# Performance work log

Measured on AMD Instinct MI355X. Metric: run time of the kernel, lower is better.

Reference implementation:

```python
import jax, jax.numpy as jnp
import numpy as np
from jax import lax

N_CLASS, SOS, EOS, NEG = 5, 0, 4, -10000.0


def _lstm_dir(x, Wih, Whh, bih, bhh, reverse):
    # x: (T, B, Din); PyTorch gate order i, f, g, o
    T, B, _ = x.shape
    Hd = Whh.shape[1]
    h0 = jnp.zeros((B, Hd), x.dtype)

    def step(carry, xt):
        h, c = carry
        g = xt @ Wih.T + h @ Whh.T + bih + bhh
        i, f, gg, o = jnp.split(g, 4, axis=-1)
        c = jax.nn.sigmoid(f) * c + jax.nn.sigmoid(i) * jnp.tanh(gg)
        h = jax.nn.sigmoid(o) * jnp.tanh(c)
        return (h, c), h

    xs = x[::-1] if reverse else x
    _, hs = lax.scan(step, (h0, h0), xs)
    return hs[::-1] if reverse else hs


def _forward(input_ids, tags, mask, emb, convs, lstm_params, lin_w, lin_b, transition):
    T, B = mask.shape
    x = emb[input_ids][:, None]  # (N, 1, L, E)
    pooled = []
    for w, b in convs:  # w: (K, 1, size, E)
        c = lax.conv_general_dilated(x, w, (1, 1), 'VALID',
                                     dimension_numbers=('NCHW', 'OIHW', 'NCHW'))
        c = jax.nn.relu(c[..., 0] + b[None, :, None])  # (N, K, L-size+1)
        pooled.append(jnp.max(c, axis=2))              # max-pool over length
    para = jnp.concatenate(pooled, axis=1)             # (N, 3K)
    h = para.reshape(B, T, -1).transpose(1, 0, 2)      # (T, B, 3K); equal para_len
    for (Wf, Uf, bf, cf, Wb, Ub, bb, cb) in lstm_params:  # 2-layer BiLSTM (eval: no dropout)
        hf = _lstm_dir(h, Wf, Uf, bf, cf, False)
        hb = _lstm_dir(h, Wb, Ub, bb, cb, True)
        h = jnp.concatenate([hf, hb], axis=-1)
    m = mask[..., None]
    feats = ((h * m) @ lin_w.T + lin_b) * m            # (T, B, 5)

    # CRF forward algorithm (log partition)
    alpha0 = jnp.full((B, N_CLASS), NEG, feats.dtype).at[:, SOS].set(0.0)

    def step(alpha, inp):
        feat, mt = inp
        s = alpha[:, None, :] + transition[None] + feat[:, :, None]
        new = jax.nn.logsumexp(s, axis=-1)
        return new * mt[:, None] + alpha * (1.0 - mt[:, None]), None

    alpha, _ = lax.scan(step, alpha0, (feats, mask))
    fwd_score = jax.nn.logsumexp(alpha + transition[EOS][None], axis=-1)

    # gold path score
    tags_ext = jnp.concatenate([jnp.full((1, B), SOS, tags.dtype), tags], 0)  # (T+1, B)
    emit = jnp.take_along_axis(feats, tags[..., None], axis=-1)[..., 0]       # (T, B)
    trans = transition[tags_ext[1:], tags_ext[:-1]]                           # (T, B)
    gold = jnp.sum((emit + trans) * mask, axis=0)
    lengths = mask.sum(0).astype(jnp.int32)
    last = tags_ext[lengths, jnp.arange(B)]
    gold = gold + transition[EOS, last]
    return (fwd_score - gold).sum()


def setup_inputs() -> dict:
    key = jax.random.key(0)
    ks = jax.random.split(key, 32)
    B, T, L, V, E, K, H = 8, 64, 64, 50000, 768, 256, 64
    N = B * T
    inp = {}
    inp['input_ids'] = jax.random.randint(ks[0], (N, L), 1, V)
    inp['tags'] = jax.random.randint(ks[1], (T, B), 1, 4)  # B/I/O tags
    inp['mask'] = jnp.ones((T, B), jnp.float32)
    inp['para_len'] = jnp.full((B,), T, jnp.int32)
    inp['emb'] = jax.random.normal(ks[2], (V, E)) * 0.1
    for i, sz in enumerate((3, 4, 5)):
        inp[f'cw{sz}'] = jax.random.normal(ks[3 + i], (K, 1, sz, E)) * (1.0 / np.sqrt(sz * E))
        inp[f'cb{sz}'] = jnp.zeros((K,), jnp.float32)
    kidx = 6
    for layer, din in ((0, 3 * K), (1, 2 * H)):
        for d in 'fb':
            inp[f'Wih{layer}{d}'] = jax.random.normal(ks[kidx], (4 * H, din)) * (1.0 / np.sqrt(din)); kidx += 1
            inp[f'Whh{layer}{d}'] = jax.random.normal(ks[kidx], (4 * H, H)) * (1.0 / np.sqrt(H)); kidx += 1
            inp[f'bih{layer}{d}'] = jnp.zeros((4 * H,), jnp.float32)
            inp[f'bhh{layer}{d}'] = jnp.zeros((4 * H,), jnp.float32)
    inp['lin_w'] = jax.random.normal(ks[kidx], (N_CLASS, 2 * H)) * 0.1; kidx += 1
    inp['lin_b'] = jnp.zeros((N_CLASS,), jnp.float32)
    tr = jax.random.normal(ks[kidx], (N_CLASS, N_CLASS))
    inp['transition'] = tr.at[SOS, :].set(NEG).at[:, EOS].set(NEG)
    return inp


def reference(input_ids, tags, mask, para_len, emb, cw3, cb3, cw4, cb4, cw5, cb5,
              Wih0f, Whh0f, bih0f, bhh0f, Wih0b, Whh0b, bih0b, bhh0b,
              Wih1f, Whh1f, bih1f, bhh1f, Wih1b, Whh1b, bih1b, bhh1b,
              lin_w, lin_b, transition):
    convs = ((cw3, cb3), (cw4, cb4), (cw5, cb5))
    lstm_params = ((Wih0f, Whh0f, bih0f, bhh0f, Wih0b, Whh0b, bih0b, bhh0b),
                   (Wih1f, Whh1f, bih1f, bhh1f, Wih1b, Whh1b, bih1b, bhh1b))
    return _forward(input_ids, tags, mask, emb, convs, lstm_params, lin_w, lin_b, transition)
```

## Files before the change

### kernel.cpp

```cpp
#include <hip/hip_runtime.h>
#include <cstdint>
#include <cstddef>

#define DEV __device__ __forceinline__

typedef __bf16 bf16x8 __attribute__((ext_vector_type(8)));
typedef float f32x4 __attribute__((ext_vector_type(4)));

#define NEG_VAL -10000.0f

DEV unsigned int f2bf(float f) {
    unsigned int u = __float_as_uint(f);
    return (u + 0x7FFFu + ((u >> 16) & 1u)) >> 16;
}
DEV unsigned int pk2(float a, float b) { return f2bf(a) | (f2bf(b) << 16); }

DEV float sigf(float x)  { return __builtin_amdgcn_rcpf(1.f + __expf(-x)); }
DEV float tanhff(float x){ return 2.f * __builtin_amdgcn_rcpf(1.f + __expf(-2.f * x)) - 1.f; }

__global__ void cast_all_kernel(const float* __restrict__ cw3,
                                const float* __restrict__ cw4,
                                const float* __restrict__ cw5,
                                const float* __restrict__ Wih0f,
                                const float* __restrict__ Wih0b,
                                const float* __restrict__ Wih1f,
                                const float* __restrict__ Wih1b,
                                unsigned short* __restrict__ wbc,
                                unsigned short* __restrict__ wih0c,
                                unsigned short* __restrict__ wih1c) {
    int tid = blockIdx.x * blockDim.x + threadIdx.x;
    const float* src;
    uint4* dstp;
    if (tid < 294912) {
        int g   = tid & 3;
        int col = (tid >> 2) & 255;
        int c   = (tid >> 10) % 24;
        int p   = tid / (24 * 256 * 4);
        int sz, j; const float* W;
        if (p < 3)      { sz = 3; j = p;     W = cw3; }
        else if (p < 7) { sz = 4; j = p - 3; W = cw4; }
        else            { sz = 5; j = p - 7; W = cw5; }
        src = W + ((size_t)col * sz + j) * 768 + c * 32 + g * 8;
        dstp = reinterpret_cast<uint4*>(wbc) +
               ((size_t)(p * 24 + c) * 1024 + (col >> 4) * 64 + g * 16 + (col & 15));
    } else if (tid < 294912 + 49152) {
        int u   = tid - 294912;
        int g   = u & 3;
        int col = (u >> 2) & 255;
        int kc  = (u >> 10) % 24;
        int dir = u / (24 * 256 * 4);
        const float* W = dir ? Wih0b : Wih0f;
        src = W + (size_t)col * 768 + kc * 32 + g * 8;
        dstp = reinterpret_cast<uint4*>(wih0c) +
               ((size_t)(dir * 24 + kc) * 1024 + (col >> 4) * 64 + g * 16 + (col & 15));
    } else if (tid < 294912 + 49152 + 8192) {
        int u   = tid - 294912 - 49152;
        int g   = u & 3;
        int col = (u >> 2) & 255;
        int kc  = (u >> 10) % 4;
        int dir = u / (4 * 256 * 4);
        const float* W = dir ? Wih1b : Wih1f;
        src = W + (size_t)col * 128 + kc * 32 + g * 8;
        dstp = reinterpret_cast<uint4*>(wih1c) +
               ((size_t)(dir * 4 + kc) * 1024 + (col >> 4) * 64 + g * 16 + (col & 15));
    } else return;
    float4 a = *(const float4*)(src);
    float4 b = *(const float4*)(src + 4);
    *dstp = make_uint4(pk2(a.x, a.y), pk2(a.z, a.w), pk2(b.x, b.y), pk2(b.z, b.w));
}

template<int SZ>
DEV void conv_body(const int* __restrict__ ids,
                   const float* __restrict__ emb,
                   const unsigned short* __restrict__ wbc,
                   const float* __restrict__ cb,
                   unsigned short* __restrict__ para_bf,
                   int pair, int szi, int pbase,
                   unsigned short* Xlds)
{
    int tid  = threadIdx.x;
    int lane = tid & 63;
    int nw   = tid >> 6;
    int l15  = lane & 15;
    int q    = lane >> 4;
    int n0   = pair * 2;

    int srow  = tid >> 1;
    int shalf = tid & 1;
    int sid   = ids[(n0 + (srow >> 6)) * 64 + (srow & 63)];
    const float* embrow = emb + (size_t)sid * 768 + shalf * 16;
    int skey = (srow >> 1) & 3;
    int xo0 = srow * 32 + (((2 * shalf)     ^ skey) * 8);
    int xo1 = srow * 32 + (((2 * shalf + 1) ^ skey) * 8);

    int vlaneB = nw * 2048 + lane * 8;

    f32x4 acc[8][4];
    #pragma unroll
    for (int a = 0; a < 8; a++)
        #pragma unroll
        for (int t = 0; t < 4; t++) acc[a][t] = (f32x4){0.f, 0.f, 0.f, 0.f};

    bf16x8 bfr[2][4];
    float4 e0, e1, e2, e3;

    {
        e0 = ((const float4*)embrow)[0];
        e1 = ((const float4*)embrow)[1];
        e2 = ((const float4*)embrow)[2];
        e3 = ((const float4*)embrow)[3];
        const unsigned short* bt = wbc + (size_t)(pbase * 24) * 8192 + vlaneB;
        #pragma unroll
        for (int t = 0; t < 4; t++)
            bfr[0][t] = *(const bf16x8*)(bt + t * 512);
        uint4 p0 = make_uint4(pk2(e0.x, e0.y), pk2(e0.z, e0.w),
                              pk2(e1.x, e1.y), pk2(e1.z, e1.w));
        uint4 p1 = make_uint4(pk2(e2.x, e2.y), pk2(e2.z, e2.w),
                              pk2(e3.x, e3.y), pk2(e3.z, e3.w));
        *(uint4*)&Xlds[xo0] = p0;
        *(uint4*)&Xlds[xo1] = p1;
        asm volatile("s_waitcnt lgkmcnt(0)" ::: "memory");
        __builtin_amdgcn_s_barrier();
    }

    int cbase = pbase * 24;
    for (int c2 = 0; c2 < 24; c2 += 2, cbase += 2) {
        #pragma unroll
        for (int s2 = 0; s2 < 2 * SZ; ++s2) {
            const int half = (s2 < SZ) ? 0 : 1;
            const int j    = s2 - half * SZ;
            const int par  = s2 & 1;
            {
                const int sP = s2 + 1;
                const int offP = (sP < SZ) ? sP * 24
                               : (sP < 2 * SZ ? (sP - SZ) * 24 + 1 : 2);
                const unsigned short* bt =
                    wbc + (size_t)(cbase + offP) * 8192 + vlaneB;
                #pragma unroll
                for (int t = 0; t < 4; t++)
                    bfr[par ^ 1][t] = *(const bf16x8*)(bt + t * 512);
            }
            if (s2 == 0 || s2 == SZ) {
                int cE = half ? c2 + 2 : c2 + 1; if (cE > 23) cE = 0;
                const float* sp = embrow + cE * 32;
                e0 = ((const float4*)sp)[0];
                e1 = ((const float4*)sp)[1];
                e2 = ((const float4*)sp)[2];
                e3 = ((const float4*)sp)[3];
            }

            const unsigned short* Xb = Xlds + half * 4096;
            {
                bf16x8 af[4];
                #pragma unroll
                for (int a = 0; a < 4; a++) {
                    int pp = 16 * a + l15 + j; if (pp > 63) pp = 63;
                    af[a] = *(const bf16x8*)(
                        &Xb[pp * 32 + ((q ^ ((pp >> 1) & 3)) * 8)]);
                }
                __builtin_amdgcn_s_setprio(1);
                #pragma unroll
                for (int a = 0; a < 4; a++)
                    #pragma unroll
                    for (int t = 0; t < 4; t++)
                        acc[a][t] = __builtin_amdgcn_mfma_f32_16x16x32_bf16(
                            af[a], bfr[par][t], acc[a][t], 0, 0, 0);
                __builtin_amdgcn_s_setprio(0);
            }
            {
                bf16x8 af[4];
                #pragma unroll
                for (int a = 0; a < 4; a++) {
                    int pp = 16 * a + l15 + j; if (pp > 63) pp = 63;
                    int xr = 64 + pp;
                    af[a] = *(const bf16x8*)(
                        &Xb[xr * 32 + ((q ^ ((xr >> 1) & 3)) * 8)]);
                }
                __builtin_amdgcn_s_setprio(1);
                #pragma unroll
                for (int a = 0; a < 4; a++)
                    #pragma unroll
                    for (int t = 0; t < 4; t++)
                        acc[4 + a][t] = __builtin_amdgcn_mfma_f32_16x16x32_bf16(
                            af[a], bfr[par][t], acc[4 + a][t], 0, 0, 0);
                __builtin_amdgcn_s_setprio(0);
            }

            if (j == SZ - 1) {
                unsigned short* Xw = Xlds + (half ^ 1) * 4096;
                uint4 p0 = make_uint4(pk2(e0.x, e0.y), pk2(e0.z, e0.w),
                                      pk2(e1.x, e1.y), pk2(e1.z, e1.w));
                uint4 p1 = make_uint4(pk2(e2.x, e2.y), pk2(e2.z, e2.w),
                                      pk2(e3.x, e3.y), pk2(e3.z, e3.w));
                *(uint4*)&Xw[xo0] = p0;
                *(uint4*)&Xw[xo1] = p1;
                asm volatile("s_waitcnt lgkmcnt(0)" ::: "memory");
                __builtin_amdgcn_s_barrier();
            }
        }
    }

    int pmax = 64 - SZ;
    #pragma unroll
    for (int t = 0; t < 4; t++) {
        int colb = nw * 64 + t * 16;
        float bias = cb[colb + l15];
        #pragma unroll
        for (int s = 0; s < 2; s++) {
            float m = 0.0f;
            #pragma unroll
            for (int a4 = 0; a4 < 4; a4++) {
                #pragma unroll
                for (int r = 0; r < 4; r++) {
                    int p = 16 * a4 + q * 4 + r;
                    float v = acc[s * 4 + a4][t][r] + bias;
                    v = v > 0.f ? v : 0.f;
                    if (p <= pmax) m = v > m ? v : m;
                }
            }
            m = fmaxf(m, __shfl_xor(m, 16));
            m = fmaxf(m, __shfl_xor(m, 32));
            if (lane < 16) {
                int n = n0 + s;
                int row = (n & 63) * 8 + (n >> 6);
                para_bf[(size_t)row * 768 + szi * 256 + colb + lane] =
                    (unsigned short)f2bf(m);
            }
        }
    }
}

__global__ __launch_bounds__(256, 2) void conv_pool_kernel(
    const int* __restrict__ ids,
    const float* __restrict__ emb,
    const unsigned short* __restrict__ wbc,
    const float* __restrict__ cb3, const float* __restrict__ cb4,
    const float* __restrict__ cb5,
    unsigned short* __restrict__ para_bf)
{
    __shared__ unsigned short Xlds[2][4096];
    int bx   = blockIdx.x;
    int szi  = bx >> 8;
    int pair = bx & 255;
    if (szi == 0)
        conv_body<3>(ids, emb, wbc, cb3, para_bf, pair, 0, 0, &Xlds[0][0]);
    else if (szi == 1)
        conv_body<4>(ids, emb, wbc, cb4, para_bf, pair, 1, 3, &Xlds[0][0]);
    else
        conv_body<5>(ids, emb, wbc, cb5, para_bf, pair, 2, 7, &Xlds[0][0]);
}

template<int KC>
__global__ __launch_bounds__(256) void gemm_in_kernel(
    const unsigned short* __restrict__ xbf,
    const unsigned short* __restrict__ wihc,
    const float* __restrict__ bihF, const float* __restrict__ bhhF,
    const float* __restrict__ bihB, const float* __restrict__ bhhB,
    float* __restrict__ gates)
{
    const int din = KC * 32;
    int bx   = blockIdx.x;
    int dir  = bx >> 3;
    int rowg = (bx >> 1) & 3;
    int colg = bx & 1;
    int tid  = threadIdx.x;
    int lane = tid & 63;
    int wid  = tid >> 6;
    int mw   = wid >> 1;
    int nw   = wid & 1;
    int l15  = lane & 15;
    int q    = lane >> 4;

    const float* bih = dir ? bihB : bihF;
    const float* bhh = dir ? bhhB : bhhF;
    const unsigned short* wt = wihc + (size_t)dir * KC * 8192;

    const unsigned short* arow[4];
    #pragma unroll
    for (int a = 0; a < 4; a++)
        arow[a] = xbf + (size_t)(rowg * 128 + mw * 64 + a * 16 + l15) * din + q * 8;
    const unsigned short* bbase = wt + (colg * 8 + nw * 4) * 512 + lane * 8;

    f32x4 acc[4][4];
    #pragma unroll
    for (int a = 0; a < 4; a++)
        #pragma unroll
        for (int t = 0; t < 4; t++) acc[a][t] = (f32x4){0.f, 0.f, 0.f, 0.f};

    bf16x8 afb[2][4], bfb[2][4];
    #pragma unroll
    for (int a = 0; a < 4; a++) afb[0][a] = *(const bf16x8*)(arow[a]);
    #pragma unroll
    for (int t = 0; t < 4; t++) bfb[0][t] = *(const bf16x8*)(bbase + t * 512);

    #pragma unroll 2
    for (int kc = 0; kc < KC; ++kc) {
        const int p = kc & 1;
        int kn = (kc + 1 < KC) ? kc + 1 : kc;
        #pragma unroll
        for (int a = 0; a < 4; a++)
            afb[p ^ 1][a] = *(const bf16x8*)(arow[a] + kn * 32);
        #pragma unroll
        for (int t = 0; t < 4; t++)
            bfb[p ^ 1][t] = *(const bf16x8*)(bbase + (size_t)kn * 8192 + t * 512);
        __builtin_amdgcn_s_setprio(1);
        #pragma unroll
        for (int a = 0; a < 4; a++)
            #pragma unroll
            for (int t = 0; t < 4; t++)
                acc[a][t] = __builtin_amdgcn_mfma_f32_16x16x32_bf16(
                    afb[p][a], bfb[p][t], acc[a][t], 0, 0, 0);
        __builtin_amdgcn_s_setprio(0);
    }

    #pragma unroll
    for (int t = 0; t < 4; t++) {
        int nn = colg * 128 + nw * 64 + t * 16 + l15;
        float bb = bih[nn] + bhh[nn];
        float* gp = gates + ((size_t)dir * 256 + nn) * 512 +
                    rowg * 128 + mw * 64 + q * 4;
        #pragma unroll
        for (int a = 0; a < 4; a++) {
            f32x4 v = acc[a][t];
            v[0] += bb; v[1] += bb; v[2] += bb; v[3] += bb;
            *(f32x4*)(gp + a * 16) = v;
        }
    }
}

__global__ __launch_bounds__(256) void lstm_rec_kernel(
    const float* __restrict__ gates,
    const float* __restrict__ WhhF, const float* __restrict__ WhhB,
    float* __restrict__ houtF,
    unsigned short* __restrict__ houtB)
{
    int dir = blockIdx.x;
    const float* Whh = dir ? WhhB : WhhF;
    const float* gin = gates + (size_t)dir * 256 * 512;

    __shared__ unsigned short h16[2][16 * 64];

    int tid  = threadIdx.x;
    int lane = tid & 63;
    int w    = tid >> 6;
    int l15  = lane & 15;
    int q    = lane >> 4;
    int hh   = 16 * w + l15;

    bf16x8 Bf[4][2];
    #pragma unroll
    for (int g = 0; g < 4; g++)
        #pragma unroll
        for (int kh = 0; kh < 2; kh++) {
            const float* wp = Whh + (size_t)(g * 64 + hh) * 64 + kh * 32 + q * 8;
            float4 f0 = *(const float4*)wp;
            float4 f1 = *(const float4*)(wp + 4);
            bf16x8 r;
            r[0] = (__bf16)f0.x; r[1] = (__bf16)f0.y;
            r[2] = (__bf16)f0.z; r[3] = (__bf16)f0.w;
            r[4] = (__bf16)f1.x; r[5] = (__bf16)f1.y;
            r[6] = (__bf16)f1.z; r[7] = (__bf16)f1.w;
            Bf[g][kh] = r;
        }

    const float* pg0 = gin + ((size_t)(0 * 64 + hh)) * 512 + 4 * (q & 1);
    const float* pg1 = gin + ((size_t)(1 * 64 + hh)) * 512 + 4 * (q & 1);
    const float* pg2 = gin + ((size_t)(2 * 64 + hh)) * 512 + 4 * (q & 1);
    const float* pg3 = gin + ((size_t)(3 * 64 + hh)) * 512 + 4 * (q & 1);

    for (int i = tid; i < 2 * 16 * 64; i += 256)
        ((unsigned short*)h16)[i] = 0;
    float cst[4] = {0.f, 0.f, 0.f, 0.f};
    __syncthreads();

    int t0 = dir ? 63 : 0;
    f32x4 gv0 = *(const f32x4*)(pg0 + t0 * 8);
    f32x4 gv1 = *(const f32x4*)(pg1 + t0 * 8);
    f32x4 gv2 = *(const f32x4*)(pg2 + t0 * 8);
    f32x4 gv3 = *(const f32x4*)(pg3 + t0 * 8);

    for (int s = 0; s < 64; ++s) {
        int t = dir ? 63 - s : s;
        const unsigned short* hb = h16[s & 1];
        int slot0 = q ^ (l15 & 7);
        int slot1 = (4 + q) ^ (l15 & 7);
        bf16x8 a0 = *(const bf16x8*)&hb[l15 * 64 + slot0 * 8];
        bf16x8 a1 = *(const bf16x8*)&hb[l15 * 64 + slot1 * 8];

        f32x4 zero = (f32x4){0.f, 0.f, 0.f, 0.f};
        f32x4 acc[4];
        #pragma unroll
        for (int g = 0; g < 4; g++) {
            acc[g] = __builtin_amdgcn_mfma_f32_16x16x32_bf16(a0, Bf[g][0], zero, 0, 0, 0);
            acc[g] = __builtin_amdgcn_mfma_f32_16x16x32_bf16(a1, Bf[g][1], acc[g], 0, 0, 0);
        }

        int sn = (s + 1 < 64) ? s + 1 : 63;
        int t2 = dir ? 63 - sn : sn;
        f32x4 n0 = *(const f32x4*)(pg0 + t2 * 8);
        f32x4 n1 = *(const f32x4*)(pg1 + t2 * 8);
        f32x4 n2 = *(const f32x4*)(pg2 + t2 * 8);
        f32x4 n3 = *(const f32x4*)(pg3 + t2 * 8);

        if (q < 2) {
            unsigned short* hw = h16[(s + 1) & 1];
            #pragma unroll
            for (int r = 0; r < 4; r++) {
                int b = 4 * q + r;
                float gi = acc[0][r] + gv0[r];
                float gf = acc[1][r] + gv1[r];
                float gg = acc[2][r] + gv2[r];
                float go = acc[3][r] + gv3[r];
                float cn = sigf(gf) * cst[r] + sigf(gi) * tanhff(gg);
                float hv = sigf(go) * tanhff(cn);
                cst[r] = cn;
                int slot = (hh >> 3) ^ (b & 7);
                hw[b * 64 + slot * 8 + (hh & 7)] = (unsigned short)f2bf(hv);
                size_t oi = ((size_t)t * 8 + b) * 128 + dir * 64 + hh;
                if (houtF) houtF[oi] = hv;
                houtB[oi] = (unsigned short)f2bf(hv);
            }
        }
        __syncthreads();
        gv0 = n0; gv1 = n1; gv2 = n2; gv3 = n3;
    }
}

__global__ __launch_bounds__(512) void crf_kernel(
    const float* __restrict__ h1,
    const float* __restrict__ lin_w,
    const float* __restrict__ lin_b,
    const float* __restrict__ mask,
    const int* __restrict__ tags,
    const float* __restrict__ trans,
    float* __restrict__ out) {
    __shared__ float feats[64][8][5];
    __shared__ float wl[5][128];
    __shared__ float msk[512];
    __shared__ int   tgs[512];
    __shared__ float fwd_s[8], gold_s[8];
    __shared__ float tr[25], trE[5], lb[5];
    int tid = threadIdx.x;
    if (tid < 25) tr[tid] = trans[tid];
    if (tid < 5) { trE[tid] = trans[20 + tid]; lb[tid] = lin_b[tid]; }
    msk[tid] = mask[tid];
    tgs[tid] = tags[tid];
    if (tid < 128) {
        #pragma unroll
        for (int i = 0; i < 5; i++) wl[i][tid] = lin_w[i * 128 + tid];
    }
    __syncthreads();

    {
        const float4* h4 = (const float4*)(h1 + (size_t)tid * 128);
        float a0 = 0.f, a1 = 0.f, a2 = 0.f, a3 = 0.f, a4 = 0.f;
        for (int e4 = 0; e4 < 32; e4++) {
            float4 hv = h4[e4];
            int e = e4 * 4;
            a0 += hv.x * wl[0][e] + hv.y * wl[0][e+1] + hv.z * wl[0][e+2] + hv.w * wl[0][e+3];
            a1 += hv.x * wl[1][e] + hv.y * wl[1][e+1] + hv.z * wl[1][e+2] + hv.w * wl[1][e+3];
            a2 += hv.x * wl[2][e] + hv.y * wl[2][e+1] + hv.z * wl[2][e+2] + hv.w * wl[2][e+3];
            a3 += hv.x * wl[3][e] + hv.y * wl[3][e+1] + hv.z * wl[3][e+2] + hv.w * wl[3][e+3];
            a4 += hv.x * wl[4][e] + hv.y * wl[4][e+1] + hv.z * wl[4][e+2] + hv.w * wl[4][e+3];
        }
        float m = msk[tid];
        int t = tid >> 3, b = tid & 7;
        feats[t][b][0] = (m * a0 + lb[0]) * m;
        feats[t][b][1] = (m * a1 + lb[1]) * m;
        feats[t][b][2] = (m * a2 + lb[2]) * m;
        feats[t][b][3] = (m * a3 + lb[3]) * m;
        feats[t][b][4] = (m * a4 + lb[4]) * m;
    }
    __syncthreads();

    if (tid < 40) {
        int b = tid / 5, i = tid % 5;
        float alpha = (i == 0) ? 0.f : NEG_VAL;
        float trow[5];
        #pragma unroll
        for (int j2 = 0; j2 < 5; j2++) trow[j2] = tr[i * 5 + j2];
        for (int t = 0; t < 64; t++) {
            float s0, s1, s2, s3, s4;
            s0 = __shfl(alpha, b * 5 + 0, 64) + trow[0];
            s1 = __shfl(alpha, b * 5 + 1, 64) + trow[1];
            s2 = __shfl(alpha, b * 5 + 2, 64) + trow[2];
            s3 = __shfl(alpha, b * 5 + 3, 64) + trow[3];
            s4 = __shfl(alpha, b * 5 + 4, 64) + trow[4];
            float mx = fmaxf(fmaxf(fmaxf(s0, s1), fmaxf(s2, s3)), s4);
            float sum = expf(s0 - mx) + expf(s1 - mx) + expf(s2 - mx) +
                        expf(s3 - mx) + expf(s4 - mx);
            float lse = mx + logf(sum) + feats[t][b][i];
            float mt = msk[t * 8 + b];
            alpha = mt * lse + (1.f - mt) * alpha;
        }
        float v = alpha + trE[i];
        float m0 = __shfl(v, b * 5 + 0, 64);
        float m1 = __shfl(v, b * 5 + 1, 64);
        float m2 = __shfl(v, b * 5 + 2, 64);
        float m3 = __shfl(v, b * 5 + 3, 64);
        float m4 = __shfl(v, b * 5 + 4, 64);
        float mx = fmaxf(fmaxf(fmaxf(m0, m1), fmaxf(m2, m3)), m4);
        float sum = expf(m0 - mx) + expf(m1 - mx) + expf(m2 - mx) +
                    expf(m3 - mx) + expf(m4 - mx);
        if (i == 0) fwd_s[b] = mx + logf(sum);
    }
    if (tid >= 64 && tid < 72) {
        int b = tid - 64;
        float g = 0.f, lenf = 0.f;
        int prev = 0;
        for (int t = 0; t < 64; t++) {
            int tg = tgs[t * 8 + b];
            float mt = msk[t * 8 + b];
            g += (feats[t][b][tg] + tr[tg * 5 + prev]) * mt;
            lenf += mt;
            prev = tg;
        }
        int len = (int)lenf;
        int last = (len == 0) ? 0 : tgs[(len - 1) * 8 + b];
        g += trE[last];
        gold_s[b] = g;
    }
    __syncthreads();
    if (tid == 0) {
        float s = 0.f;
        for (int b = 0; b < 8; b++) s += fwd_s[b] - gold_s[b];
        out[0] = s;
    }
}

extern "C" void kernel_launch(void* const* d_in, const int* in_sizes, int n_in,
                              void* d_out, int out_size, void* d_ws, size_t ws_size,
                              hipStream_t stream) {
    const int*   ids   = (const int*)d_in[0];
    const int*   tags  = (const int*)d_in[1];
    const float* mask  = (const float*)d_in[2];
    const float* emb   = (const float*)d_in[4];
    const float* cw3   = (const float*)d_in[5];
    const float* cb3   = (const float*)d_in[6];
    const float* cw4   = (const float*)d_in[7];
    const float* cb4   = (const float*)d_in[8];
    const float* cw5   = (const float*)d_in[9];
    const float* cb5   = (const float*)d_in[10];
    const float* Wih0f = (const float*)d_in[11];
    const float* Whh0f = (const float*)d_in[12];
    const float* bih0f = (const float*)d_in[13];
    const float* bhh0f = (const float*)d_in[14];
    const float* Wih0b = (const float*)d_in[15];
    const float* Whh0b = (const float*)d_in[16];
    const float* bih0b = (const float*)d_in[17];
    const float* bhh0b = (const float*)d_in[18];
    const float* Wih1f = (const float*)d_in[19];
    const float* Whh1f = (const float*)d_in[20];
    const float* bih1f = (const float*)d_in[21];
    const float* bhh1f = (const float*)d_in[22];
    const float* Wih1b = (const float*)d_in[23];
    const float* Whh1b = (const float*)d_in[24];
    const float* bih1b = (const float*)d_in[25];
    const float* bhh1b = (const float*)d_in[26];
    const float* lin_w = (const float*)d_in[27];
    const float* lin_b = (const float*)d_in[28];
    const float* trans = (const float*)d_in[29];

    char* ws = (char*)d_ws;
    unsigned short* wbc     = (unsigned short*)ws;
    unsigned short* wih0c   = (unsigned short*)(ws + 4718592);
    unsigned short* wih1c   = (unsigned short*)(ws + 5505024);
    unsigned short* para_bf = (unsigned short*)(ws + 5636096);
    float*          gates   = (float*)(ws + 6422528);
    unsigned short* h0_bf   = (unsigned short*)(ws + 5636096);
    float*          h1f     = (float*)(ws + 4718592);

    hipLaunchKernelGGL(cast_all_kernel, dim3(1376), dim3(256), 0, stream,
                       cw3, cw4, cw5, Wih0f, Wih0b, Wih1f, Wih1b,
                       wbc, wih0c, wih1c);
    hipLaunchKernelGGL(conv_pool_kernel, dim3(768), dim3(256), 0, stream,
                       ids, emb, wbc, cb3, cb4, cb5, para_bf);
    hipLaunchKernelGGL((gemm_in_kernel<24>), dim3(16), dim3(256), 0, stream,
                       para_bf, wih0c, bih0f, bhh0f, bih0b, bhh0b, gates);
    hipLaunchKernelGGL(lstm_rec_kernel, dim3(2), dim3(256), 0, stream,
                       gates, Whh0f, Whh0b, (float*)nullptr, h0_bf);
    hipLaunchKernelGGL((gemm_in_kernel<4>), dim3(16), dim3(256), 0, stream,
                       h0_bf, wih1c, bih1f, bhh1f, bih1b, bhh1b, gates);
    hipLaunchKernelGGL(lstm_rec_kernel, dim3(2), dim3(256), 0, stream,
                       gates, Whh1f, Whh1b, h1f, h0_bf);
    hipLaunchKernelGGL(crf_kernel, dim3(1), dim3(512), 0, stream,
                       h1f, lin_w, lin_b, mask, tags, trans, (float*)d_out);
}
```

Before: 283.0 us.

## Software-pipeline conv LDS fragment reads and double gemm_in grid

In the conv kernel, the A-fragment LDS reads are split into pairs and prefetched one stage ahead, so they overlap the MFMAs instead of stalling before each group of 16. The LDS buffer is padded with zeroed rows, which removes the per-row clamp on out-of-range positions. The input-projection GEMM now uses 64-row tiles, doubling the grid from 16 to 32 blocks for more parallelism on a small launch, and its setprio hints are dropped. The cost is more register pressure in the conv kernel and less data reuse per block in the GEMM.

```diff
diff --git a/kernel.cpp b/kernel.cpp
--- a/kernel.cpp
+++ b/kernel.cpp
@@ -69,6 +69,8 @@
     *dstp = make_uint4(pk2(a.x, a.y), pk2(a.z, a.w), pk2(b.x, b.y), pk2(b.z, b.w));
 }
 
+#define XROWS 4224
+
 template<int SZ>
 DEV void conv_body(const int* __restrict__ ids,
                    const float* __restrict__ emb,
@@ -102,7 +104,22 @@
         for (int t = 0; t < 4; t++) acc[a][t] = (f32x4){0.f, 0.f, 0.f, 0.f};
 
     bf16x8 bfr[2][4];
+    bf16x8 afb[2][2];
     float4 e0, e1, e2, e3;
+
+    if (tid < 128) {
+        ((unsigned short*)Xlds)[128 * 32 + tid] = 0;
+        ((unsigned short*)Xlds)[XROWS + 128 * 32 + tid] = 0;
+    }
+
+    auto rd2 = [&](bf16x8 (&dst)[2], const unsigned short* base,
+                   int j, int a0, int rowoff) {
+        #pragma unroll
+        for (int r = 0; r < 2; r++) {
+            int xr = rowoff + 16 * (a0 + r) + l15 + j;
+            dst[r] = *(const bf16x8*)(&base[xr * 32 + ((q ^ ((xr >> 1) & 3)) * 8)]);
+        }
+    };
 
     {
         e0 = ((const float4*)embrow)[0];
@@ -121,6 +138,7 @@
         *(uint4*)&Xlds[xo1] = p1;
         asm volatile("s_waitcnt lgkmcnt(0)" ::: "memory");
         __builtin_amdgcn_s_barrier();
+        rd2(afb[0], Xlds, 0, 0, 0);
     }
 
     int cbase = pbase * 24;
@@ -149,45 +167,43 @@
                 e3 = ((const float4*)sp)[3];
             }
 
-            const unsigned short* Xb = Xlds + half * 4096;
-            {
-                bf16x8 af[4];
-                #pragma unroll
-                for (int a = 0; a < 4; a++) {
-                    int pp = 16 * a + l15 + j; if (pp > 63) pp = 63;
-                    af[a] = *(const bf16x8*)(
-                        &Xb[pp * 32 + ((q ^ ((pp >> 1) & 3)) * 8)]);
-                }
-                __builtin_amdgcn_s_setprio(1);
-                #pragma unroll
-                for (int a = 0; a < 4; a++)
-                    #pragma unroll
-                    for (int t = 0; t < 4; t++)
-                        acc[a][t] = __builtin_amdgcn_mfma_f32_16x16x32_bf16(
-                            af[a], bfr[par][t], acc[a][t], 0, 0, 0);
-                __builtin_amdgcn_s_setprio(0);
-            }
-            {
-                bf16x8 af[4];
-                #pragma unroll
-                for (int a = 0; a < 4; a++) {
-                    int pp = 16 * a + l15 + j; if (pp > 63) pp = 63;
-                    int xr = 64 + pp;
-                    af[a] = *(const bf16x8*)(
-                        &Xb[xr * 32 + ((q ^ ((xr >> 1) & 3)) * 8)]);
-                }
-                __builtin_amdgcn_s_setprio(1);
-                #pragma unroll
-                for (int a = 0; a < 4; a++)
-                    #pragma unroll
-                    for (int t = 0; t < 4; t++)
-                        acc[4 + a][t] = __builtin_amdgcn_mfma_f32_16x16x32_bf16(
-                            af[a], bfr[par][t], acc[4 + a][t], 0, 0, 0);
-                __builtin_amdgcn_s_setprio(0);
+            const unsigned short* Xb = Xlds + half * XROWS;
+            rd2(afb[1], Xb, j, 2, 0);
+            #pragma unroll
+            for (int t = 0; t < 4; t++) {
+                acc[0][t] = __builtin_amdgcn_mfma_f32_16x16x32_bf16(
+                    afb[0][0], bfr[par][t], acc[0][t], 0, 0, 0);
+                acc[1][t] = __builtin_amdgcn_mfma_f32_16x16x32_bf16(
+                    afb[0][1], bfr[par][t], acc[1][t], 0, 0, 0);
+            }
+            rd2(afb[0], Xb, j, 0, 64);
+            #pragma unroll
+            for (int t = 0; t < 4; t++) {
+                acc[2][t] = __builtin_amdgcn_mfma_f32_16x16x32_bf16(
+                    afb[1][0], bfr[par][t], acc[2][t], 0, 0, 0);
+                acc[3][t] = __builtin_amdgcn_mfma_f32_16x16x32_bf16(
+                    afb[1][1], bfr[par][t], acc[3][t], 0, 0, 0);
+            }
+            rd2(afb[1], Xb, j, 2, 64);
+            #pragma unroll
+            for (int t = 0; t < 4; t++) {
+                acc[4][t] = __builtin_amdgcn_mfma_f32_16x16x32_bf16(
+                    afb[0][0], bfr[par][t], acc[4][t], 0, 0, 0);
+                acc[5][t] = __builtin_amdgcn_mfma_f32_16x16x32_bf16(
+                    afb[0][1], bfr[par][t], acc[5][t], 0, 0, 0);
+            }
+            if (j < SZ - 1)
+                rd2(afb[0], Xb, j + 1, 0, 0);
+            #pragma unroll
+            for (int t = 0; t < 4; t++) {
+                acc[6][t] = __builtin_amdgcn_mfma_f32_16x16x32_bf16(
+                    afb[1][0], bfr[par][t], acc[6][t], 0, 0, 0);
+                acc[7][t] = __builtin_amdgcn_mfma_f32_16x16x32_bf16(
+                    afb[1][1], bfr[par][t], acc[7][t], 0, 0, 0);
             }
 
             if (j == SZ - 1) {
-                unsigned short* Xw = Xlds + (half ^ 1) * 4096;
+                unsigned short* Xw = Xlds + (half ^ 1) * XROWS;
                 uint4 p0 = make_uint4(pk2(e0.x, e0.y), pk2(e0.z, e0.w),
                                       pk2(e1.x, e1.y), pk2(e1.z, e1.w));
                 uint4 p1 = make_uint4(pk2(e2.x, e2.y), pk2(e2.z, e2.w),
@@ -196,6 +212,7 @@
                 *(uint4*)&Xw[xo1] = p1;
                 asm volatile("s_waitcnt lgkmcnt(0)" ::: "memory");
                 __builtin_amdgcn_s_barrier();
+                rd2(afb[0], Xlds + (half ^ 1) * XROWS, 0, 0, 0);
             }
         }
     }
@@ -238,7 +255,7 @@
     const float* __restrict__ cb5,
     unsigned short* __restrict__ para_bf)
 {
-    __shared__ unsigned short Xlds[2][4096];
+    __shared__ unsigned short Xlds[2][XROWS];
     int bx   = blockIdx.x;
     int szi  = bx >> 8;
     int pair = bx & 255;
@@ -260,8 +277,8 @@
 {
     const int din = KC * 32;
     int bx   = blockIdx.x;
-    int dir  = bx >> 3;
-    int rowg = (bx >> 1) & 3;
+    int dir  = bx >> 4;
+    int rowg = (bx >> 1) & 7;
     int colg = bx & 1;
     int tid  = threadIdx.x;
     int lane = tid & 63;
@@ -275,21 +292,21 @@
     const float* bhh = dir ? bhhB : bhhF;
     const unsigned short* wt = wihc + (size_t)dir * KC * 8192;
 
-    const unsigned short* arow[4];
-    #pragma unroll
-    for (int a = 0; a < 4; a++)
-        arow[a] = xbf + (size_t)(rowg * 128 + mw * 64 + a * 16 + l15) * din + q * 8;
+    const unsigned short* arow[2];
+    #pragma unroll
+    for (int a = 0; a < 2; a++)
+        arow[a] = xbf + (size_t)(rowg * 64 + mw * 32 + a * 16 + l15) * din + q * 8;
     const unsigned short* bbase = wt + (colg * 8 + nw * 4) * 512 + lane * 8;
 
-    f32x4 acc[4][4];
-    #pragma unroll
-    for (int a = 0; a < 4; a++)
+    f32x4 acc[2][4];
+    #pragma unroll
+    for (int a = 0; a < 2; a++)
         #pragma unroll
         for (int t = 0; t < 4; t++) acc[a][t] = (f32x4){0.f, 0.f, 0.f, 0.f};
 
-    bf16x8 afb[2][4], bfb[2][4];
-    #pragma unroll
-    for (int a = 0; a < 4; a++) afb[0][a] = *(const bf16x8*)(arow[a]);
+    bf16x8 afb[2][2], bfb[2][4];
+    #pragma unroll
+    for (int a = 0; a < 2; a++) afb[0][a] = *(const bf16x8*)(arow[a]);
     #pragma unroll
     for (int t = 0; t < 4; t++) bfb[0][t] = *(const bf16x8*)(bbase + t * 512);
 
@@ -298,19 +315,17 @@
         const int p = kc & 1;
         int kn = (kc + 1 < KC) ? kc + 1 : kc;
         #pragma unroll
-        for (int a = 0; a < 4; a++)
+        for (int a = 0; a < 2; a++)
             afb[p ^ 1][a] = *(const bf16x8*)(arow[a] + kn * 32);
         #pragma unroll
         for (int t = 0; t < 4; t++)
             bfb[p ^ 1][t] = *(const bf16x8*)(bbase + (size_t)kn * 8192 + t * 512);
-        __builtin_amdgcn_s_setprio(1);
-        #pragma unroll
-        for (int a = 0; a < 4; a++)
+        #pragma unroll
+        for (int a = 0; a < 2; a++)
             #pragma unroll
             for (int t = 0; t < 4; t++)
                 acc[a][t] = __builtin_amdgcn_mfma_f32_16x16x32_bf16(
                     afb[p][a], bfb[p][t], acc[a][t], 0, 0, 0);
-        __builtin_amdgcn_s_setprio(0);
     }
 
     #pragma unroll
@@ -318,9 +333,9 @@
         int nn = colg * 128 + nw * 64 + t * 16 + l15;
         float bb = bih[nn] + bhh[nn];
         float* gp = gates + ((size_t)dir * 256 + nn) * 512 +
-                    rowg * 128 + mw * 64 + q * 4;
-        #pragma unroll
-        for (int a = 0; a < 4; a++) {
+                    rowg * 64 + mw * 32 + q * 4;
+        #pragma unroll
+        for (int a = 0; a < 2; a++) {
             f32x4 v = acc[a][t];
             v[0] += bb; v[1] += bb; v[2] += bb; v[3] += bb;
             *(f32x4*)(gp + a * 16) = v;
@@ -575,11 +590,11 @@
                        wbc, wih0c, wih1c);
     hipLaunchKernelGGL(conv_pool_kernel, dim3(768), dim3(256), 0, stream,
                        ids, emb, wbc, cb3, cb4, cb5, para_bf);
-    hipLaunchKernelGGL((gemm_in_kernel<24>), dim3(16), dim3(256), 0, stream,
+    hipLaunchKernelGGL((gemm_in_kernel<24>), dim3(32), dim3(256), 0, stream,
                        para_bf, wih0c, bih0f, bhh0f, bih0b, bhh0b, gates);
     hipLaunchKernelGGL(lstm_rec_kernel, dim3(2), dim3(256), 0, stream,
                        gates, Whh0f, Whh0b, (float*)nullptr, h0_bf);
-    hipLaunchKernelGGL((gemm_in_kernel<4>), dim3(16), dim3(256), 0, stream,
+    hipLaunchKernelGGL((gemm_in_kernel<4>), dim3(32), dim3(256), 0, stream,
                        h0_bf, wih1c, bih1f, bhh1f, bih1b, bhh1b, gates);
     hipLaunchKernelGGL(lstm_rec_kernel, dim3(2), dim3(256), 0, stream,
                        gates, Whh1f, Whh1b, h1f, h0_bf);
```

New measurement: 284.7 us. No clear change (+0.6%).
